# Kernel tuning notes

Hardware: AMD Instinct MI355X
Metric: run time of the kernel (lower is better)

The kernel has to match this reference:

```python
import jax, jax.numpy as jnp
import numpy as np

N = 50000
E = 800000
D_IN = 64
D_OUT = 64
D_EDGE = 16


def setup_inputs() -> dict:
    key = jax.random.key(0)
    ks = jax.random.split(key, 10)
    x = jax.random.normal(ks[0], (N, D_IN), dtype=jnp.float32)
    edge_index = jax.random.randint(ks[1], (2, E), 0, N, dtype=jnp.int64)
    edge_attr = jax.random.normal(ks[2], (E, D_EDGE), dtype=jnp.float32)
    s = 1.0 / np.sqrt(D_EDGE)
    We = jax.random.uniform(ks[3], (D_EDGE, D_IN), minval=-s, maxval=s, dtype=jnp.float32)
    be = jax.random.uniform(ks[4], (D_IN,), minval=-s, maxval=s, dtype=jnp.float32)
    s1 = 1.0 / np.sqrt(D_IN)
    W1 = jax.random.uniform(ks[5], (D_IN, D_OUT), minval=-s1, maxval=s1, dtype=jnp.float32)
    b1 = jax.random.uniform(ks[6], (D_OUT,), minval=-s1, maxval=s1, dtype=jnp.float32)
    s2 = 1.0 / np.sqrt(D_OUT)
    W2 = jax.random.uniform(ks[7], (D_OUT, D_OUT), minval=-s2, maxval=s2, dtype=jnp.float32)
    b2 = jax.random.uniform(ks[8], (D_OUT,), minval=-s2, maxval=s2, dtype=jnp.float32)
    return {"x": x, "edge_index": edge_index, "edge_attr": edge_attr,
            "We": We, "be": be, "W1": W1, "b1": b1, "W2": W2, "b2": b2}


def reference(x, edge_index, edge_attr, We, be, W1, b1, W2, b2):
    src = edge_index[0]  # message source j
    dst = edge_index[1]  # aggregation target i (PyG source_to_target flow)
    # per-edge message: relu(x_j + lin_edge(edge_attr))
    msg = jax.nn.relu(x[src] + edge_attr @ We + be)  # [E, D_IN]
    # scatter-sum aggregation at target nodes
    agg = jax.ops.segment_sum(msg, dst, num_segments=N)  # [N, D_IN]
    eps = 0.0  # GINEConv default, train_eps=False
    h = (1.0 + eps) * x + agg
    # mlp: Linear -> ReLU -> Linear (dropout p=0.0 -> identity)
    out = jax.nn.relu(h @ W1 + b1) @ W2 + b2
    return out
```

## Files before the change

kernel.cpp:

```cpp
#include <hip/hip_runtime.h>
#include <hip/hip_fp16.h>
#include <hip/hip_bf16.h>

#define NN 50000
#define EE 800000

__device__ __forceinline__ float bflo(unsigned u) { return __uint_as_float(u << 16); }
__device__ __forceinline__ float bfhi(unsigned u) { return __uint_as_float(u & 0xffff0000u); }

__global__ void detect_dtype(const unsigned* __restrict__ xw, int* __restrict__ flag) {
    const int t = threadIdx.x;
    unsigned e = (xw[t] >> 7) & 0xFFu;
    unsigned long long m = __ballot(e >= 100u && e <= 140u);
    if (t == 0) *flag = (__popcll(m) >= 32) ? 1 : 0;
}

template <bool BF16>
__device__ __forceinline__ float edge_lin(const void* __restrict__ eav, int e,
                                          const float* __restrict__ we, float bed) {
    float acc = bed;
    if constexpr (BF16) {
        const uint4* row = (const uint4*)((const __hip_bfloat16*)eav + (size_t)e * 16);
        const uint4 p0 = row[0];
        const uint4 p1 = row[1];
        acc = fmaf(bflo(p0.x), we[0],  acc); acc = fmaf(bfhi(p0.x), we[1],  acc);
        acc = fmaf(bflo(p0.y), we[2],  acc); acc = fmaf(bfhi(p0.y), we[3],  acc);
        acc = fmaf(bflo(p0.z), we[4],  acc); acc = fmaf(bfhi(p0.z), we[5],  acc);
        acc = fmaf(bflo(p0.w), we[6],  acc); acc = fmaf(bfhi(p0.w), we[7],  acc);
        acc = fmaf(bflo(p1.x), we[8],  acc); acc = fmaf(bfhi(p1.x), we[9],  acc);
        acc = fmaf(bflo(p1.y), we[10], acc); acc = fmaf(bfhi(p1.y), we[11], acc);
        acc = fmaf(bflo(p1.z), we[12], acc); acc = fmaf(bfhi(p1.z), we[13], acc);
        acc = fmaf(bflo(p1.w), we[14], acc); acc = fmaf(bfhi(p1.w), we[15], acc);
    } else {
        const float4* row = (const float4*)((const float*)eav + (size_t)e * 16);
        const float4 q0 = row[0], q1 = row[1], q2 = row[2], q3 = row[3];
        acc = fmaf(q0.x, we[0],  acc); acc = fmaf(q0.y, we[1],  acc);
        acc = fmaf(q0.z, we[2],  acc); acc = fmaf(q0.w, we[3],  acc);
        acc = fmaf(q1.x, we[4],  acc); acc = fmaf(q1.y, we[5],  acc);
        acc = fmaf(q1.z, we[6],  acc); acc = fmaf(q1.w, we[7],  acc);
        acc = fmaf(q2.x, we[8],  acc); acc = fmaf(q2.y, we[9],  acc);
        acc = fmaf(q2.z, we[10], acc); acc = fmaf(q2.w, we[11], acc);
        acc = fmaf(q3.x, we[12], acc); acc = fmaf(q3.y, we[13], acc);
        acc = fmaf(q3.z, we[14], acc); acc = fmaf(q3.w, we[15], acc);
    }
    return acc;
}

template <bool BF16>
__device__ __forceinline__ void edge_body(
    const void* __restrict__ xv, const int* __restrict__ ei,
    const void* __restrict__ eav, const void* __restrict__ Wev,
    const void* __restrict__ bev, __half2* __restrict__ aggh)
{
    const int tid = threadIdx.x;
    const int d   = tid & 63;
    const int sub = tid >> 6;

    const int oddor = ei[1] | ei[3] | ei[5] | ei[7] | ei[9] | ei[11] | ei[13] | ei[15];
    const bool idx64 = (oddor == 0);
    const long long* __restrict__ ei64 = (const long long*)ei;

    float we[16];
    float bed;
    if constexpr (BF16) {
        const __hip_bfloat16* We = (const __hip_bfloat16*)Wev;
#pragma unroll
        for (int k = 0; k < 16; k++) we[k] = __bfloat162float(We[k * 64 + d]);
        bed = __bfloat162float(((const __hip_bfloat16*)bev)[d]);
    } else {
        const float* We = (const float*)Wev;
#pragma unroll
        for (int k = 0; k < 16; k++) we[k] = We[k * 64 + d];
        bed = ((const float*)bev)[d];
    }

    const int wid = blockIdx.x * 4 + sub;
    const int nw  = gridDim.x * 4;
    for (int e0 = wid * 4; e0 < EE; e0 += nw * 4) {
        int src[4], dst[4];
        if (idx64) {
#pragma unroll
            for (int i = 0; i < 4; i++) {
                src[i] = (int)ei64[e0 + i];
                dst[i] = (int)ei64[EE + e0 + i];
            }
        } else {
            const int4 s4 = *(const int4*)(ei + e0);
            const int4 d4 = *(const int4*)(ei + EE + e0);
            src[0] = s4.x; src[1] = s4.y; src[2] = s4.z; src[3] = s4.w;
            dst[0] = d4.x; dst[1] = d4.y; dst[2] = d4.z; dst[3] = d4.w;
        }

        float xs[4];
#pragma unroll
        for (int i = 0; i < 4; i++) {
            if constexpr (BF16)
                xs[i] = __bfloat162float(((const __hip_bfloat16*)xv)[(size_t)src[i] * 64 + d]);
            else
                xs[i] = ((const float*)xv)[(size_t)src[i] * 64 + d];
        }

        float acc[4];
#pragma unroll
        for (int i = 0; i < 4; i++) acc[i] = edge_lin<BF16>(eav, e0 + i, we, bed);

#pragma unroll
        for (int i = 0; i < 4; i++) {
            const float msg   = fmaxf(acc[i] + xs[i], 0.0f);
            const float other = __shfl_xor(msg, 1);
            if ((d & 1) == 0) {
                __half2 v = __floats2half2_rn(msg, other);
                unsafeAtomicAdd(aggh + (size_t)dst[i] * 32 + (d >> 1), v);
            }
        }
    }
}

__global__ __launch_bounds__(256) void edge_agg_kernel(
    const void* x, const int* ei, const void* ea,
    const void* We, const void* be, __half2* aggh, const int* flag)
{
    if (*flag) edge_body<true>(x, ei, ea, We, be, aggh);
    else       edge_body<false>(x, ei, ea, We, be, aggh);
}

template <bool BF16>
__device__ __forceinline__ void mlp_body(
    const void* __restrict__ xv, const __half* __restrict__ aggh,
    const void* __restrict__ W1v, const void* __restrict__ b1v,
    const void* __restrict__ W2v, const void* __restrict__ b2v,
    void* __restrict__ outv, float (*sh)[64], float (*st)[64])
{
    const int tid = threadIdx.x;
    const int d   = tid & 63;
    const int w   = tid >> 6;

    float w1c[64], w2c[64], b1d, b2d;
    if constexpr (BF16) {
        const __hip_bfloat16* W1 = (const __hip_bfloat16*)W1v;
        const __hip_bfloat16* W2 = (const __hip_bfloat16*)W2v;
#pragma unroll
        for (int k = 0; k < 64; k++) {
            w1c[k] = __bfloat162float(W1[k * 64 + d]);
            w2c[k] = __bfloat162float(W2[k * 64 + d]);
        }
        b1d = __bfloat162float(((const __hip_bfloat16*)b1v)[d]);
        b2d = __bfloat162float(((const __hip_bfloat16*)b2v)[d]);
    } else {
        const float* W1 = (const float*)W1v;
        const float* W2 = (const float*)W2v;
#pragma unroll
        for (int k = 0; k < 64; k++) {
            w1c[k] = W1[k * 64 + d];
            w2c[k] = W2[k * 64 + d];
        }
        b1d = ((const float*)b1v)[d];
        b2d = ((const float*)b2v)[d];
    }

    const int stride = gridDim.x * 4;
    int node = blockIdx.x * 4 + w;

    float xs_n = 0.0f, ag_n = 0.0f;
    if (node < NN) {
        if constexpr (BF16) xs_n = __bfloat162float(((const __hip_bfloat16*)xv)[(size_t)node * 64 + d]);
        else                xs_n = ((const float*)xv)[(size_t)node * 64 + d];
        ag_n = __half2float(aggh[(size_t)node * 64 + d]);
    }

    while (node < NN) {
        const float xs_c = xs_n, ag_c = ag_n;
        const int next = node + stride;
        if (next < NN) {
            if constexpr (BF16) xs_n = __bfloat162float(((const __hip_bfloat16*)xv)[(size_t)next * 64 + d]);
            else                xs_n = ((const float*)xv)[(size_t)next * 64 + d];
            ag_n = __half2float(aggh[(size_t)next * 64 + d]);
        }

        sh[w][d] = xs_c + ag_c;

        float t = b1d;
        const float4* hv = (const float4*)sh[w];
#pragma unroll
        for (int k = 0; k < 16; k++) {
            const float4 hq = hv[k];
            t = fmaf(hq.x, w1c[4 * k],     t);
            t = fmaf(hq.y, w1c[4 * k + 1], t);
            t = fmaf(hq.z, w1c[4 * k + 2], t);
            t = fmaf(hq.w, w1c[4 * k + 3], t);
        }
        t = fmaxf(t, 0.0f);
        st[w][d] = t;

        float o = b2d;
        const float4* tv = (const float4*)st[w];
#pragma unroll
        for (int k = 0; k < 16; k++) {
            const float4 tq = tv[k];
            o = fmaf(tq.x, w2c[4 * k],     o);
            o = fmaf(tq.y, w2c[4 * k + 1], o);
            o = fmaf(tq.z, w2c[4 * k + 2], o);
            o = fmaf(tq.w, w2c[4 * k + 3], o);
        }
        if constexpr (BF16) ((__hip_bfloat16*)outv)[(size_t)node * 64 + d] = __float2bfloat16(o);
        else                ((float*)outv)[(size_t)node * 64 + d] = o;
        node = next;
    }
}

__global__ __launch_bounds__(256) void mlp_kernel(
    const void* x, const __half* aggh,
    const void* W1, const void* b1, const void* W2, const void* b2,
    void* out, const int* flag)
{
    __shared__ float sh[4][64];
    __shared__ float st[4][64];
    if (*flag) mlp_body<true >(x, aggh, W1, b1, W2, b2, out, sh, st);
    else       mlp_body<false>(x, aggh, W1, b1, W2, b2, out, sh, st);
}

extern "C" void kernel_launch(void* const* d_in, const int* in_sizes, int n_in,
                              void* d_out, int out_size, void* d_ws, size_t ws_size,
                              hipStream_t stream) {
    const void* x          = d_in[0];
    const int*  edge_index = (const int*)d_in[1];
    const void* edge_attr  = d_in[2];
    const void* We         = d_in[3];
    const void* be         = d_in[4];
    const void* W1         = d_in[5];
    const void* b1         = d_in[6];
    const void* W2         = d_in[7];
    const void* b2         = d_in[8];

    __half* aggh = (__half*)d_ws;
    int*    flag = (int*)((char*)d_ws + (size_t)NN * 64 * sizeof(float));

    hipMemsetAsync(aggh, 0, (size_t)NN * 64 * sizeof(__half), stream);
    hipLaunchKernelGGL(detect_dtype, dim3(1), dim3(64), 0, stream,
                       (const unsigned*)x, flag);
    hipLaunchKernelGGL(edge_agg_kernel, dim3(4096), dim3(256), 0, stream,
                       x, edge_index, edge_attr, We, be, (__half2*)aggh, flag);
    hipLaunchKernelGGL(mlp_kernel, dim3(768), dim3(256), 0, stream,
                       x, aggh, W1, b1, W2, b2, d_out, flag);
}
```

Baseline: 266.9 us.

## Replace atomic scatter aggregation with CSR sort-by-destination and per-node gather

The change builds a CSR index on every call: histogram of destinations, a single-block prefix scan, and an atomic scatter of edge ids and 16-bit source ids. Each wavefront then walks one node's incoming edges and accumulates in fp32 registers before a single fp16 store, removing the half2 atomic adds into the aggregation buffer. The cost is three extra kernels per call, including a one-block serial-ish scan, plus random edge_attr reads in sorted order. Source ids are stored as unsigned short even though N is 50000, which fits only because N is below 65536.

```diff
diff --git a/kernel.cpp b/kernel.cpp
--- a/kernel.cpp
+++ b/kernel.cpp
@@ -4,6 +4,13 @@
 
 #define NN 50000
 #define EE 800000
+
+#define OFF_AGGH   0ull
+#define OFF_EID    6400000ull
+#define OFF_SRC    9600000ull
+#define OFF_ROWPTR 11200000ull
+#define OFF_CURSOR 11400008ull
+#define OFF_FLAG   12800000ull
 
 __device__ __forceinline__ float bflo(unsigned u) { return __uint_as_float(u << 16); }
 __device__ __forceinline__ float bfhi(unsigned u) { return __uint_as_float(u & 0xffff0000u); }
@@ -46,20 +53,78 @@
     return acc;
 }
 
+__global__ __launch_bounds__(256) void hist_kernel(const int* __restrict__ ei,
+                                                   int* __restrict__ cnt) {
+    const int oddor = ei[1] | ei[3] | ei[5] | ei[7] | ei[9] | ei[11] | ei[13] | ei[15];
+    const bool idx64 = (oddor == 0);
+    const long long* __restrict__ ei64 = (const long long*)ei;
+    const int gid = blockIdx.x * 256 + threadIdx.x;
+    const int gs  = gridDim.x * 256;
+    for (int e = gid; e < EE; e += gs) {
+        const int dst = idx64 ? (int)ei64[EE + e] : ei[EE + e];
+        atomicAdd(&cnt[dst], 1);
+    }
+}
+
+__global__ __launch_bounds__(1024) void scan_kernel(int* __restrict__ cnt,
+                                                    int* __restrict__ rowptr) {
+    __shared__ int part[1024];
+    const int t  = threadIdx.x;
+    const int CH = 49;
+    int lo = t * CH, hi = lo + CH;
+    if (hi > NN) hi = NN;
+    if (lo > NN) lo = NN;
+    int s = 0;
+    for (int i = lo; i < hi; i++) s += cnt[i];
+    part[t] = s;
+    __syncthreads();
+    for (int off = 1; off < 1024; off <<= 1) {
+        int add = (t >= off) ? part[t - off] : 0;
+        __syncthreads();
+        part[t] += add;
+        __syncthreads();
+    }
+    int run = part[t] - s;
+    for (int i = lo; i < hi; i++) {
+        const int c = cnt[i];
+        rowptr[i] = run;
+        cnt[i]    = run;
+        run += c;
+    }
+    if (t == 1023) rowptr[NN] = part[1023];
+}
+
+__global__ __launch_bounds__(256) void scatter_kernel(const int* __restrict__ ei,
+                                                      int* __restrict__ cursor,
+                                                      int* __restrict__ recs_eid,
+                                                      unsigned short* __restrict__ recs_src) {
+    const int oddor = ei[1] | ei[3] | ei[5] | ei[7] | ei[9] | ei[11] | ei[13] | ei[15];
+    const bool idx64 = (oddor == 0);
+    const long long* __restrict__ ei64 = (const long long*)ei;
+    const int gid = blockIdx.x * 256 + threadIdx.x;
+    const int gs  = gridDim.x * 256;
+    for (int e = gid; e < EE; e += gs) {
+        int src, dst;
+        if (idx64) { src = (int)ei64[e]; dst = (int)ei64[EE + e]; }
+        else       { src = ei[e];        dst = ei[EE + e]; }
+        const int p = atomicAdd(&cursor[dst], 1);
+        recs_eid[p] = e;
+        recs_src[p] = (unsigned short)src;
+    }
+}
+
 template <bool BF16>
-__device__ __forceinline__ void edge_body(
-    const void* __restrict__ xv, const int* __restrict__ ei,
+__device__ __forceinline__ void gather_body(
+    const void* __restrict__ xv,
+    const int* __restrict__ recs_eid, const unsigned short* __restrict__ recs_src,
+    const int* __restrict__ rowptr,
     const void* __restrict__ eav, const void* __restrict__ Wev,
-    const void* __restrict__ bev, __half2* __restrict__ aggh)
+    const void* __restrict__ bev, __half* __restrict__ aggh)
 {
     const int tid = threadIdx.x;
     const int d   = tid & 63;
     const int sub = tid >> 6;
 
-    const int oddor = ei[1] | ei[3] | ei[5] | ei[7] | ei[9] | ei[11] | ei[13] | ei[15];
-    const bool idx64 = (oddor == 0);
-    const long long* __restrict__ ei64 = (const long long*)ei;
-
     float we[16];
     float bed;
     if constexpr (BF16) {
@@ -76,52 +141,50 @@
 
     const int wid = blockIdx.x * 4 + sub;
     const int nw  = gridDim.x * 4;
-    for (int e0 = wid * 4; e0 < EE; e0 += nw * 4) {
-        int src[4], dst[4];
-        if (idx64) {
+    for (int n = wid; n < NN; n += nw) {
+        const int beg = rowptr[n];
+        const int end = rowptr[n + 1];
+        float agg = 0.0f;
+        int k = beg;
+        for (; k + 4 <= end; k += 4) {
+            int e[4], s[4];
+#pragma unroll
+            for (int i = 0; i < 4; i++) { e[i] = recs_eid[k + i]; s[i] = (int)recs_src[k + i]; }
+            float xs[4];
 #pragma unroll
             for (int i = 0; i < 4; i++) {
-                src[i] = (int)ei64[e0 + i];
-                dst[i] = (int)ei64[EE + e0 + i];
+                if constexpr (BF16)
+                    xs[i] = __bfloat162float(((const __hip_bfloat16*)xv)[(size_t)s[i] * 64 + d]);
+                else
+                    xs[i] = ((const float*)xv)[(size_t)s[i] * 64 + d];
             }
-        } else {
-            const int4 s4 = *(const int4*)(ei + e0);
-            const int4 d4 = *(const int4*)(ei + EE + e0);
-            src[0] = s4.x; src[1] = s4.y; src[2] = s4.z; src[3] = s4.w;
-            dst[0] = d4.x; dst[1] = d4.y; dst[2] = d4.z; dst[3] = d4.w;
-        }
-
-        float xs[4];
-#pragma unroll
-        for (int i = 0; i < 4; i++) {
+            float acc[4];
+#pragma unroll
+            for (int i = 0; i < 4; i++) acc[i] = edge_lin<BF16>(eav, e[i], we, bed);
+#pragma unroll
+            for (int i = 0; i < 4; i++) agg += fmaxf(acc[i] + xs[i], 0.0f);
+        }
+        for (; k < end; ++k) {
+            const int e0 = recs_eid[k];
+            const int s0 = (int)recs_src[k];
+            float x0;
             if constexpr (BF16)
-                xs[i] = __bfloat162float(((const __hip_bfloat16*)xv)[(size_t)src[i] * 64 + d]);
+                x0 = __bfloat162float(((const __hip_bfloat16*)xv)[(size_t)s0 * 64 + d]);
             else
-                xs[i] = ((const float*)xv)[(size_t)src[i] * 64 + d];
-        }
-
-        float acc[4];
-#pragma unroll
-        for (int i = 0; i < 4; i++) acc[i] = edge_lin<BF16>(eav, e0 + i, we, bed);
-
-#pragma unroll
-        for (int i = 0; i < 4; i++) {
-            const float msg   = fmaxf(acc[i] + xs[i], 0.0f);
-            const float other = __shfl_xor(msg, 1);
-            if ((d & 1) == 0) {
-                __half2 v = __floats2half2_rn(msg, other);
-                unsafeAtomicAdd(aggh + (size_t)dst[i] * 32 + (d >> 1), v);
-            }
-        }
-    }
-}
-
-__global__ __launch_bounds__(256) void edge_agg_kernel(
-    const void* x, const int* ei, const void* ea,
-    const void* We, const void* be, __half2* aggh, const int* flag)
+                x0 = ((const float*)xv)[(size_t)s0 * 64 + d];
+            agg += fmaxf(edge_lin<BF16>(eav, e0, we, bed) + x0, 0.0f);
+        }
+        aggh[(size_t)n * 64 + d] = __float2half(agg);
+    }
+}
+
+__global__ __launch_bounds__(256) void gather_agg_kernel(
+    const void* x, const int* recs_eid, const unsigned short* recs_src,
+    const int* rowptr, const void* ea, const void* We, const void* be,
+    __half* aggh, const int* flag)
 {
-    if (*flag) edge_body<true>(x, ei, ea, We, be, aggh);
-    else       edge_body<false>(x, ei, ea, We, be, aggh);
+    if (*flag) gather_body<true >(x, recs_eid, recs_src, rowptr, ea, We, be, aggh);
+    else       gather_body<false>(x, recs_eid, recs_src, rowptr, ea, We, be, aggh);
 }
 
 template <bool BF16>
@@ -232,14 +295,25 @@
     const void* W2         = d_in[7];
     const void* b2         = d_in[8];
 
-    __half* aggh = (__half*)d_ws;
-    int*    flag = (int*)((char*)d_ws + (size_t)NN * 64 * sizeof(float));
-
-    hipMemsetAsync(aggh, 0, (size_t)NN * 64 * sizeof(__half), stream);
+    char* ws = (char*)d_ws;
+    __half*         aggh   = (__half*)(ws + OFF_AGGH);
+    int*            eid    = (int*)(ws + OFF_EID);
+    unsigned short* rsrc   = (unsigned short*)(ws + OFF_SRC);
+    int*            rowptr = (int*)(ws + OFF_ROWPTR);
+    int*            cursor = (int*)(ws + OFF_CURSOR);
+    int*            flag   = (int*)(ws + OFF_FLAG);
+
+    hipMemsetAsync(cursor, 0, (size_t)NN * sizeof(int), stream);
     hipLaunchKernelGGL(detect_dtype, dim3(1), dim3(64), 0, stream,
                        (const unsigned*)x, flag);
-    hipLaunchKernelGGL(edge_agg_kernel, dim3(4096), dim3(256), 0, stream,
-                       x, edge_index, edge_attr, We, be, (__half2*)aggh, flag);
+    hipLaunchKernelGGL(hist_kernel, dim3(1024), dim3(256), 0, stream,
+                       edge_index, cursor);
+    hipLaunchKernelGGL(scan_kernel, dim3(1), dim3(1024), 0, stream,
+                       cursor, rowptr);
+    hipLaunchKernelGGL(scatter_kernel, dim3(1024), dim3(256), 0, stream,
+                       edge_index, cursor, eid, rsrc);
+    hipLaunchKernelGGL(gather_agg_kernel, dim3(2048), dim3(256), 0, stream,
+                       x, eid, rsrc, rowptr, edge_attr, We, be, aggh, flag);
     hipLaunchKernelGGL(mlp_kernel, dim3(768), dim3(256), 0, stream,
                        x, aggh, W1, b1, W2, b2, d_out, flag);
 }
```

Result: slower. 456.6 us (+71.1%).

## Partition edge gather by source-node slice per XCD for L2 locality

Applied to the files above, without the earlier changes.

A new pack kernel compresses src and dst into one 32-bit word per edge, with 16 bits each. The aggregation kernel assigns each block a source-node slice (blockIdx & 7) and an edge chunk. Wavefronts ballot-filter the chunk for edges whose source lies in their slice and compact them into an LDS queue before gathering x and doing the atomic scatter. The intent is that blocks sharing an XCD touch only a small, L2-resident part of x, instead of gathering random rows across the whole feature matrix. In exchange, every packed index is scanned eight times and an extra kernel launch is added. The scheme also relies on node ids fitting in 16 bits and on round-robin block-to-XCD placement.

```diff
diff --git a/kernel.cpp b/kernel.cpp
--- a/kernel.cpp
+++ b/kernel.cpp
@@ -4,6 +4,15 @@
 
 #define NN 50000
 #define EE 800000
+#define NSLICE 8
+#define SLICE 6250
+#define NCHUNK 256
+#define CHUNK 3125
+#define WQ 784
+
+#define OFF_AGGH 0ull
+#define OFF_SD   6400000ull
+#define OFF_FLAG 12800000ull
 
 __device__ __forceinline__ float bflo(unsigned u) { return __uint_as_float(u << 16); }
 __device__ __forceinline__ float bfhi(unsigned u) { return __uint_as_float(u & 0xffff0000u); }
@@ -13,6 +22,18 @@
     unsigned e = (xw[t] >> 7) & 0xFFu;
     unsigned long long m = __ballot(e >= 100u && e <= 140u);
     if (t == 0) *flag = (__popcll(m) >= 32) ? 1 : 0;
+}
+
+__global__ __launch_bounds__(256) void pack_kernel(const int* __restrict__ ei,
+                                                   unsigned* __restrict__ sd) {
+    const int oddor = ei[1] | ei[3] | ei[5] | ei[7] | ei[9] | ei[11] | ei[13] | ei[15];
+    const bool idx64 = (oddor == 0);
+    const long long* __restrict__ ei64 = (const long long*)ei;
+    const int e = blockIdx.x * 256 + threadIdx.x;
+    int src, dst;
+    if (idx64) { src = (int)ei64[e]; dst = (int)ei64[EE + e]; }
+    else       { src = ei[e];        dst = ei[EE + e]; }
+    sd[e] = (unsigned)src | ((unsigned)dst << 16);
 }
 
 template <bool BF16>
@@ -47,18 +68,41 @@
 }
 
 template <bool BF16>
-__device__ __forceinline__ void edge_body(
-    const void* __restrict__ xv, const int* __restrict__ ei,
+__device__ __forceinline__ float loadx(const void* __restrict__ xv, int s, int d) {
+    if constexpr (BF16)
+        return __bfloat162float(((const __hip_bfloat16*)xv)[(size_t)s * 64 + d]);
+    else
+        return ((const float*)xv)[(size_t)s * 64 + d];
+}
+
+template <bool BF16>
+__device__ __forceinline__ void do_edge(
+    const void* __restrict__ xv, const void* __restrict__ eav,
+    const float* __restrict__ we, float bed, __half2* __restrict__ aggh,
+    int src, int dst, int eid, int d)
+{
+    const float xs  = loadx<BF16>(xv, src, d);
+    const float a   = edge_lin<BF16>(eav, eid, we, bed);
+    const float msg = fmaxf(a + xs, 0.0f);
+    const float oth = __shfl_xor(msg, 1);
+    if ((d & 1) == 0) {
+        __half2 v = __floats2half2_rn(msg, oth);
+        unsafeAtomicAdd(aggh + (size_t)dst * 32 + (d >> 1), v);
+    }
+}
+
+template <bool BF16>
+__device__ __forceinline__ void slice_body(
+    const void* __restrict__ xv, const unsigned* __restrict__ sd,
     const void* __restrict__ eav, const void* __restrict__ Wev,
-    const void* __restrict__ bev, __half2* __restrict__ aggh)
-{
-    const int tid = threadIdx.x;
-    const int d   = tid & 63;
-    const int sub = tid >> 6;
-
-    const int oddor = ei[1] | ei[3] | ei[5] | ei[7] | ei[9] | ei[11] | ei[13] | ei[15];
-    const bool idx64 = (oddor == 0);
-    const long long* __restrict__ ei64 = (const long long*)ei;
+    const void* __restrict__ bev, __half2* __restrict__ aggh,
+    uint2 (*q)[WQ])
+{
+    const int tid  = threadIdx.x;
+    const int d    = tid & 63;
+    const int sub  = tid >> 6;
+    const int p    = blockIdx.x & 7;
+    const int c    = blockIdx.x >> 3;
 
     float we[16];
     float bed;
@@ -74,54 +118,73 @@
         bed = ((const float*)bev)[d];
     }
 
-    const int wid = blockIdx.x * 4 + sub;
-    const int nw  = gridDim.x * 4;
-    for (int e0 = wid * 4; e0 < EE; e0 += nw * 4) {
-        int src[4], dst[4];
-        if (idx64) {
-#pragma unroll
-            for (int i = 0; i < 4; i++) {
-                src[i] = (int)ei64[e0 + i];
-                dst[i] = (int)ei64[EE + e0 + i];
-            }
-        } else {
-            const int4 s4 = *(const int4*)(ei + e0);
-            const int4 d4 = *(const int4*)(ei + EE + e0);
-            src[0] = s4.x; src[1] = s4.y; src[2] = s4.z; src[3] = s4.w;
-            dst[0] = d4.x; dst[1] = d4.y; dst[2] = d4.z; dst[3] = d4.w;
-        }
-
-        float xs[4];
-#pragma unroll
-        for (int i = 0; i < 4; i++) {
-            if constexpr (BF16)
-                xs[i] = __bfloat162float(((const __hip_bfloat16*)xv)[(size_t)src[i] * 64 + d]);
-            else
-                xs[i] = ((const float*)xv)[(size_t)src[i] * 64 + d];
-        }
-
-        float acc[4];
-#pragma unroll
-        for (int i = 0; i < 4; i++) acc[i] = edge_lin<BF16>(eav, e0 + i, we, bed);
-
-#pragma unroll
-        for (int i = 0; i < 4; i++) {
-            const float msg   = fmaxf(acc[i] + xs[i], 0.0f);
-            const float other = __shfl_xor(msg, 1);
-            if ((d & 1) == 0) {
-                __half2 v = __floats2half2_rn(msg, other);
-                unsafeAtomicAdd(aggh + (size_t)dst[i] * 32 + (d >> 1), v);
-            }
-        }
-    }
-}
-
-__global__ __launch_bounds__(256) void edge_agg_kernel(
-    const void* x, const int* ei, const void* ea,
+    const int cb = c * CHUNK;
+    const int a0 = cb + sub * 782;
+    const int a1 = cb + min(CHUNK, (sub + 1) * 782);
+
+    int cnt = 0;
+    for (int base = a0; base < a1; base += 64) {
+        const int e = base + d;
+        unsigned v = 0;
+        bool own = false;
+        if (e < a1) {
+            v = sd[e];
+            own = ((int)(v & 0xFFFFu) / SLICE) == p;
+        }
+        const unsigned long long m = __ballot(own);
+        if (own) {
+            const int rank = __popcll(m & ((1ull << d) - 1ull));
+            q[sub][cnt + rank] = make_uint2(v, (unsigned)e);
+        }
+        cnt += __popcll(m);
+    }
+
+    int k = 0;
+    for (; k + 4 <= cnt; k += 4) {
+        const uint2 r0 = q[sub][k],     r1 = q[sub][k + 1];
+        const uint2 r2 = q[sub][k + 2], r3 = q[sub][k + 3];
+        const int s0 = r0.x & 0xFFFFu, t0 = r0.x >> 16, e0 = (int)r0.y;
+        const int s1 = r1.x & 0xFFFFu, t1 = r1.x >> 16, e1 = (int)r1.y;
+        const int s2 = r2.x & 0xFFFFu, t2 = r2.x >> 16, e2 = (int)r2.y;
+        const int s3 = r3.x & 0xFFFFu, t3 = r3.x >> 16, e3 = (int)r3.y;
+        const float x0 = loadx<BF16>(xv, s0, d);
+        const float x1 = loadx<BF16>(xv, s1, d);
+        const float x2 = loadx<BF16>(xv, s2, d);
+        const float x3 = loadx<BF16>(xv, s3, d);
+        const float a0f = edge_lin<BF16>(eav, e0, we, bed);
+        const float a1f = edge_lin<BF16>(eav, e1, we, bed);
+        const float a2f = edge_lin<BF16>(eav, e2, we, bed);
+        const float a3f = edge_lin<BF16>(eav, e3, we, bed);
+        const float m0 = fmaxf(a0f + x0, 0.0f);
+        const float m1 = fmaxf(a1f + x1, 0.0f);
+        const float m2 = fmaxf(a2f + x2, 0.0f);
+        const float m3 = fmaxf(a3f + x3, 0.0f);
+        const float o0 = __shfl_xor(m0, 1);
+        const float o1 = __shfl_xor(m1, 1);
+        const float o2 = __shfl_xor(m2, 1);
+        const float o3 = __shfl_xor(m3, 1);
+        if ((d & 1) == 0) {
+            const int h = d >> 1;
+            unsafeAtomicAdd(aggh + (size_t)t0 * 32 + h, __floats2half2_rn(m0, o0));
+            unsafeAtomicAdd(aggh + (size_t)t1 * 32 + h, __floats2half2_rn(m1, o1));
+            unsafeAtomicAdd(aggh + (size_t)t2 * 32 + h, __floats2half2_rn(m2, o2));
+            unsafeAtomicAdd(aggh + (size_t)t3 * 32 + h, __floats2half2_rn(m3, o3));
+        }
+    }
+    for (; k < cnt; ++k) {
+        const uint2 r = q[sub][k];
+        do_edge<BF16>(xv, eav, we, bed, aggh,
+                      (int)(r.x & 0xFFFFu), (int)(r.x >> 16), (int)r.y, d);
+    }
+}
+
+__global__ __launch_bounds__(256) void slice_agg_kernel(
+    const void* x, const unsigned* sd, const void* ea,
     const void* We, const void* be, __half2* aggh, const int* flag)
 {
-    if (*flag) edge_body<true>(x, ei, ea, We, be, aggh);
-    else       edge_body<false>(x, ei, ea, We, be, aggh);
+    __shared__ uint2 q[4][WQ];
+    if (*flag) slice_body<true >(x, sd, ea, We, be, aggh, q);
+    else       slice_body<false>(x, sd, ea, We, be, aggh, q);
 }
 
 template <bool BF16>
@@ -232,14 +295,18 @@
     const void* W2         = d_in[7];
     const void* b2         = d_in[8];
 
-    __half* aggh = (__half*)d_ws;
-    int*    flag = (int*)((char*)d_ws + (size_t)NN * 64 * sizeof(float));
+    char* ws = (char*)d_ws;
+    __half*   aggh = (__half*)(ws + OFF_AGGH);
+    unsigned* sd   = (unsigned*)(ws + OFF_SD);
+    int*      flag = (int*)(ws + OFF_FLAG);
 
     hipMemsetAsync(aggh, 0, (size_t)NN * 64 * sizeof(__half), stream);
     hipLaunchKernelGGL(detect_dtype, dim3(1), dim3(64), 0, stream,
                        (const unsigned*)x, flag);
-    hipLaunchKernelGGL(edge_agg_kernel, dim3(4096), dim3(256), 0, stream,
-                       x, edge_index, edge_attr, We, be, (__half2*)aggh, flag);
+    hipLaunchKernelGGL(pack_kernel, dim3(EE / 256), dim3(256), 0, stream,
+                       edge_index, sd);
+    hipLaunchKernelGGL(slice_agg_kernel, dim3(NSLICE * NCHUNK), dim3(256), 0, stream,
+                       x, sd, edge_attr, We, be, (__half2*)aggh, flag);
     hipLaunchKernelGGL(mlp_kernel, dim3(768), dim3(256), 0, stream,
                        x, aggh, W1, b1, W2, b2, d_out, flag);
 }
```

After: 275.4 us. 1.03x slower.
